# Performance work log

Hardware: AMD Instinct MI355X
Metric: run time of the kernel (lower is better)

The kernel has to match this reference:

```python
import jax, jax.numpy as jnp
import numpy as np

N_POI = 100000   # number of POIs
N_EDGE = 50000   # directed hyperedges
N_USER = 50000   # user hyperedges (multi-view)
NNZ = 1_000_000  # nonzeros per incidence matrix
D = 128          # embedding dim
L = 3            # num_layers


def spmm(rows, cols, vals, x, num_rows):
    """COO sparse @ dense: y[r] += vals * x[c]."""
    return jax.ops.segment_sum(vals[:, None] * x[cols], rows, num_segments=num_rows)


def hyper_net(pois, rows1, cols1, vals1, n1, rows2, cols2, vals2, n2, attn):
    """Chained two-hop sparse propagation with relu + residual, layer-attention fusion.
    Dropout omitted (eval mode / deterministic reference)."""
    embs = [pois]
    x = pois
    for _ in range(L):
        m = spmm(rows1, cols1, vals1, x, n1)      # [n1, D] aggregate to hyperedges/users
        m = spmm(rows2, cols2, vals2, m, n2)      # [N_POI, D] propagate back to POIs
        x = jax.nn.relu(m) + embs[-1]             # relu + residual
        embs.append(x)
    w = jax.nn.softmax(attn)                      # [L+1]
    return jnp.einsum('l,lnd->nd', w, jnp.stack(embs))


def setup_inputs() -> dict:
    key = jax.random.key(0)
    ks = jax.random.split(key, 16)
    inp = {
        'pois_embs': jax.random.normal(ks[0], (N_POI, D), dtype=jnp.float32),
        'tar_rows': jax.random.randint(ks[1], (NNZ,), 0, N_EDGE, dtype=jnp.int32),
        'tar_cols': jax.random.randint(ks[2], (NNZ,), 0, N_POI, dtype=jnp.int32),
        'tar_vals': jax.random.uniform(ks[3], (NNZ,), dtype=jnp.float32),
        'src_rows': jax.random.randint(ks[4], (NNZ,), 0, N_POI, dtype=jnp.int32),
        'src_cols': jax.random.randint(ks[5], (NNZ,), 0, N_EDGE, dtype=jnp.int32),
        'src_vals': jax.random.uniform(ks[6], (NNZ,), dtype=jnp.float32),
        'up_rows': jax.random.randint(ks[7], (NNZ,), 0, N_USER, dtype=jnp.int32),
        'up_cols': jax.random.randint(ks[8], (NNZ,), 0, N_POI, dtype=jnp.int32),
        'up_vals': jax.random.uniform(ks[9], (NNZ,), dtype=jnp.float32),
        'pu_rows': jax.random.randint(ks[10], (NNZ,), 0, N_POI, dtype=jnp.int32),
        'pu_cols': jax.random.randint(ks[11], (NNZ,), 0, N_USER, dtype=jnp.int32),
        'pu_vals': jax.random.uniform(ks[12], (NNZ,), dtype=jnp.float32),
        'attn_di': jnp.ones((L + 1,), dtype=jnp.float32),
        'attn_mv': jnp.ones((L + 1,), dtype=jnp.float32),
    }
    return inp


def reference(pois_embs, tar_rows, tar_cols, tar_vals, src_rows, src_cols, src_vals,
              up_rows, up_cols, up_vals, pu_rows, pu_cols, pu_vals, attn_di, attn_mv):
    # Directed hypergraph branch: msg_tar = HG_poi_tar @ x ; msg_src = HG_poi_src @ msg_tar
    di = hyper_net(pois_embs, tar_rows, tar_cols, tar_vals, N_EDGE,
                   src_rows, src_cols, src_vals, N_POI, attn_di)
    # Multi-view (user) hypergraph branch: HG_up @ x ; HG_pu @ msg
    mv = hyper_net(pois_embs, up_rows, up_cols, up_vals, N_USER,
                   pu_rows, pu_cols, pu_vals, N_POI, attn_mv)
    return di + mv
```

## Files before the change

kernel.cpp:

```cpp
#include <hip/hip_runtime.h>

#define NNZC   1000000
#define NPOI   100000
#define NEDGE  50000
#define NUSER  50000
#define DIM    128
#define NL     3

#define PB     64
#define NBKT   196
#define SCANN  (4 * NBKT * PB)

static inline int ceil_div(int a, int b) { return (a + b - 1) / b; }

typedef unsigned int uint32;

__device__ __forceinline__ float bfLO(uint32 u) { return __uint_as_float(u << 16); }
__device__ __forceinline__ float bfHI(uint32 u) { return __uint_as_float(u & 0xffff0000u); }
__device__ __forceinline__ uint32 bf16_rne(float f) {
    uint32 u = __float_as_uint(f);
    return (u + 0x7fffu + ((u >> 16) & 1u)) >> 16;
}
__device__ __forceinline__ uint32 bfPACK(float a, float b) {
    return bf16_rne(a) | (bf16_rne(b) << 16);
}
__device__ __forceinline__ uint32 csrPACK(int col, float val) {
    return ((uint32)col) | (bf16_rne(val) << 17);
}
__device__ __forceinline__ int   csrCOL(uint32 e) { return (int)(e & 0x1FFFFu); }
__device__ __forceinline__ float csrVAL(uint32 e) { return __uint_as_float((e >> 17) << 16); }

__device__ __constant__ const int c_nrows[4]  = { NEDGE, NPOI, NUSER, NPOI };
__device__ __constant__ const int c_cntoff[4] = { 0, NEDGE, NEDGE + NPOI, NEDGE + NPOI + NUSER };
__device__ __constant__ const int c_cap[4]    = { 64, 48, 64, 48 };
__device__ __constant__ const int c_shift[4]  = { 8, 9, 8, 9 };
__device__ __constant__ const long long c_elloff[4] = { 0, 3200000, 8000000, 11200000 };


__global__ __launch_bounds__(1024) void histH_kernel(
    const int* __restrict__ r0, const int* __restrict__ r1,
    const int* __restrict__ r2, const int* __restrict__ r3,
    int* __restrict__ histG) {
    __shared__ int h[NBKT];
    int m = blockIdx.y, p = blockIdx.x;
    for (int i = threadIdx.x; i < NBKT; i += 1024) h[i] = 0;
    __syncthreads();
    const int* r = (m == 0) ? r0 : (m == 1) ? r1 : (m == 2) ? r2 : r3;
    int shift = c_shift[m];
    int lo = (int)(((long long)NNZC * p) >> 6);
    int hi = (int)(((long long)NNZC * (p + 1)) >> 6);
    for (int i = lo + (int)threadIdx.x; i < hi; i += 1024)
        atomicAdd(&h[r[i] >> shift], 1);
    __syncthreads();
    for (int b = threadIdx.x; b < NBKT; b += 1024)
        histG[(m * NBKT + b) * PB + p] = h[b];
}

__global__ __launch_bounds__(256) void scan_kernel(int* __restrict__ g) {
    __shared__ int base[257];
    int t = threadIdx.x;
    const int chunk = SCANN / 256;
    int lo = t * chunk;
    int s = 0;
    for (int i = 0; i < chunk; i++) s += g[lo + i];
    base[t + 1] = s;
    __syncthreads();
    if (t == 0) {
        base[0] = 0;
        for (int i = 1; i <= 256; i++) base[i] += base[i - 1];
    }
    __syncthreads();
    int off = base[t];
    for (int i = 0; i < chunk; i++) { int v = g[lo + i]; g[lo + i] = off; off += v; }
    if (t == 255) g[SCANN] = base[256];
}

__global__ __launch_bounds__(1024) void scatS_kernel(
    const int* __restrict__ r0, const int* __restrict__ r1,
    const int* __restrict__ r2, const int* __restrict__ r3,
    const int* __restrict__ c0, const int* __restrict__ c1,
    const int* __restrict__ c2, const int* __restrict__ c3,
    const float* __restrict__ v0, const float* __restrict__ v1,
    const float* __restrict__ v2, const float* __restrict__ v3,
    const int* __restrict__ scanG, uint2* __restrict__ rec) {
    __shared__ int cur[NBKT];
    int m = blockIdx.y, p = blockIdx.x;
    for (int b = threadIdx.x; b < NBKT; b += 1024)
        cur[b] = scanG[(m * NBKT + b) * PB + p];
    __syncthreads();
    const int*   r = (m == 0) ? r0 : (m == 1) ? r1 : (m == 2) ? r2 : r3;
    const int*   c = (m == 0) ? c0 : (m == 1) ? c1 : (m == 2) ? c2 : c3;
    const float* v = (m == 0) ? v0 : (m == 1) ? v1 : (m == 2) ? v2 : v3;
    int shift = c_shift[m];
    int lo = (int)(((long long)NNZC * p) >> 6);
    int hi = (int)(((long long)NNZC * (p + 1)) >> 6);
    for (int i = lo + (int)threadIdx.x; i < hi; i += 1024) {
        int row = r[i];
        int pos = atomicAdd(&cur[row >> shift], 1);
        rec[pos] = make_uint2((uint32)row, csrPACK(c[i], v[i]));
    }
}

__global__ __launch_bounds__(512) void fillB_kernel(
    const int* __restrict__ scanG, const uint2* __restrict__ rec,
    int* __restrict__ counts_all, uint32* __restrict__ ell) {
    __shared__ int cnt[512];
    int bx = (int)blockIdx.x;
    int m = bx / NBKT, b = bx - m * NBKT;
    int shift = c_shift[m];
    int rowlo = b << shift;
    int bklen = 1 << shift;
    for (int i = threadIdx.x; i < bklen; i += 512) cnt[i] = 0;
    __syncthreads();
    int lo = scanG[(m * NBKT + b) * PB];
    int hi = scanG[(m * NBKT + b + 1) * PB];
    int cap = c_cap[m];
    uint32* ebase = ell + c_elloff[m];
    for (int i = lo + (int)threadIdx.x; i < hi; i += 512) {
        uint2 e = rec[i];
        int row = (int)e.x;
        int pos = atomicAdd(&cnt[row - rowlo], 1);
        ebase[(size_t)row * cap + pos] = e.y;
    }
    __syncthreads();
    int nrows_b = c_nrows[m] - rowlo;
    if (nrows_b > bklen) nrows_b = bklen;
    int* counts = counts_all + c_cntoff[m];
    for (int i = threadIdx.x; i < nrows_b; i += 512) {
        int ci = cnt[i];
        counts[rowlo + i] = ci;
        int pad = (ci + 7) & ~7;
        uint32* erow = ebase + (size_t)(rowlo + i) * cap;
        for (int j = ci; j < pad; j++) erow[j] = 0;
    }
}

__global__ __launch_bounds__(256) void cast_soft_kernel(
    const float* __restrict__ src, uint32* __restrict__ dst,
    const float* __restrict__ adi, const float* __restrict__ amv,
    float* __restrict__ w) {
    int bx = (int)blockIdx.x;
    if (bx < 25000) {
        int i = bx * 256 + (int)threadIdx.x;
        float2 f = *(const float2*)(src + (size_t)i * 2);
        dst[i] = bfPACK(f.x, f.y);
        return;
    }
    if (threadIdx.x == 0) {
        for (int b = 0; b < 2; b++) {
            const float* a = b ? amv : adi;
            float m = a[0];
            for (int l = 1; l < 4; l++) m = fmaxf(m, a[l]);
            float e[4]; float s = 0.f;
            for (int l = 0; l < 4; l++) { e[l] = __expf(a[l] - m); s += e[l]; }
            for (int l = 0; l < 4; l++) w[b * 4 + l] = e[l] / s;
        }
    }
}

__device__ __forceinline__ void fma8(float2& a0, float2& a1, float2& a2, float2& a3,
                                     float v, uint4 u) {
    a0.x = fmaf(v, bfLO(u.x), a0.x); a0.y = fmaf(v, bfHI(u.x), a0.y);
    a1.x = fmaf(v, bfLO(u.y), a1.x); a1.y = fmaf(v, bfHI(u.y), a1.y);
    a2.x = fmaf(v, bfLO(u.z), a2.x); a2.y = fmaf(v, bfHI(u.z), a2.y);
    a3.x = fmaf(v, bfLO(u.w), a3.x); a3.y = fmaf(v, bfHI(u.w), a3.y);
}

template<int CAP>
__global__ __launch_bounds__(256) void spmm1_kernel(
    const int* __restrict__ counts, const uint32* __restrict__ ell,
    const uint32* __restrict__ xbf, uint32* __restrict__ ybf, int n_rows) {
    int row = (int)((blockIdx.x * blockDim.x + threadIdx.x) >> 4);
    int t   = (int)(threadIdx.x & 15);
    if (row >= n_rows) return;
    int pad = (counts[row] + 7) & ~7;
    const uint32* erow = ell + (size_t)row * CAP;
    float2 a0 = {0.f,0.f}, a1 = {0.f,0.f}, a2 = {0.f,0.f}, a3 = {0.f,0.f};
    for (int j = 0; j < pad; j += 8) {
        uint4 qa = *(const uint4*)(erow + j);
        uint4 qb = *(const uint4*)(erow + j + 4);
        uint4 u0 = *((const uint4*)(xbf + (size_t)csrCOL(qa.x) * 64) + t);
        uint4 u1 = *((const uint4*)(xbf + (size_t)csrCOL(qa.y) * 64) + t);
        uint4 u2 = *((const uint4*)(xbf + (size_t)csrCOL(qa.z) * 64) + t);
        uint4 u3 = *((const uint4*)(xbf + (size_t)csrCOL(qa.w) * 64) + t);
        uint4 u4 = *((const uint4*)(xbf + (size_t)csrCOL(qb.x) * 64) + t);
        uint4 u5 = *((const uint4*)(xbf + (size_t)csrCOL(qb.y) * 64) + t);
        uint4 u6 = *((const uint4*)(xbf + (size_t)csrCOL(qb.z) * 64) + t);
        uint4 u7 = *((const uint4*)(xbf + (size_t)csrCOL(qb.w) * 64) + t);
        fma8(a0,a1,a2,a3, csrVAL(qa.x), u0); fma8(a0,a1,a2,a3, csrVAL(qa.y), u1);
        fma8(a0,a1,a2,a3, csrVAL(qa.z), u2); fma8(a0,a1,a2,a3, csrVAL(qa.w), u3);
        fma8(a0,a1,a2,a3, csrVAL(qb.x), u4); fma8(a0,a1,a2,a3, csrVAL(qb.y), u5);
        fma8(a0,a1,a2,a3, csrVAL(qb.z), u6); fma8(a0,a1,a2,a3, csrVAL(qb.w), u7);
    }
    uint4 o;
    o.x = bfPACK(a0.x, a0.y); o.y = bfPACK(a1.x, a1.y);
    o.z = bfPACK(a2.x, a2.y); o.w = bfPACK(a3.x, a3.y);
    *((uint4*)(ybf + (size_t)row * 64) + t) = o;
}

template<int CAP, int MODE>
__global__ __launch_bounds__(256) void spmm2_kernel(
    const int* __restrict__ counts, const uint32* __restrict__ ell,
    const uint32* __restrict__ mbf, const uint32* __restrict__ xinbf,
    uint32* __restrict__ xoutbf, const uint32* __restrict__ x1bf,
    const float* __restrict__ pois, const float* __restrict__ w,
    float* __restrict__ outf, int n_rows) {
    int row = (int)((blockIdx.x * blockDim.x + threadIdx.x) >> 4);
    int t   = (int)(threadIdx.x & 15);
    if (row >= n_rows) return;
    int pad = (counts[row] + 7) & ~7;
    const uint32* erow = ell + (size_t)row * CAP;
    float2 a0 = {0.f,0.f}, a1 = {0.f,0.f}, a2 = {0.f,0.f}, a3 = {0.f,0.f};
    for (int j = 0; j < pad; j += 8) {
        uint4 qa = *(const uint4*)(erow + j);
        uint4 qb = *(const uint4*)(erow + j + 4);
        uint4 u0 = *((const uint4*)(mbf + (size_t)csrCOL(qa.x) * 64) + t);
        uint4 u1 = *((const uint4*)(mbf + (size_t)csrCOL(qa.y) * 64) + t);
        uint4 u2 = *((const uint4*)(mbf + (size_t)csrCOL(qa.z) * 64) + t);
        uint4 u3 = *((const uint4*)(mbf + (size_t)csrCOL(qa.w) * 64) + t);
        uint4 u4 = *((const uint4*)(mbf + (size_t)csrCOL(qb.x) * 64) + t);
        uint4 u5 = *((const uint4*)(mbf + (size_t)csrCOL(qb.y) * 64) + t);
        uint4 u6 = *((const uint4*)(mbf + (size_t)csrCOL(qb.z) * 64) + t);
        uint4 u7 = *((const uint4*)(mbf + (size_t)csrCOL(qb.w) * 64) + t);
        fma8(a0,a1,a2,a3, csrVAL(qa.x), u0); fma8(a0,a1,a2,a3, csrVAL(qa.y), u1);
        fma8(a0,a1,a2,a3, csrVAL(qa.z), u2); fma8(a0,a1,a2,a3, csrVAL(qa.w), u3);
        fma8(a0,a1,a2,a3, csrVAL(qb.x), u4); fma8(a0,a1,a2,a3, csrVAL(qb.y), u5);
        fma8(a0,a1,a2,a3, csrVAL(qb.z), u6); fma8(a0,a1,a2,a3, csrVAL(qb.w), u7);
    }
    uint4 ui = *((const uint4*)(xinbf + (size_t)row * 64) + t);
    float x2v[8] = { bfLO(ui.x), bfHI(ui.x), bfLO(ui.y), bfHI(ui.y),
                     bfLO(ui.z), bfHI(ui.z), bfLO(ui.w), bfHI(ui.w) };
    float x3v[8] = { fmaxf(a0.x,0.f)+x2v[0], fmaxf(a0.y,0.f)+x2v[1],
                     fmaxf(a1.x,0.f)+x2v[2], fmaxf(a1.y,0.f)+x2v[3],
                     fmaxf(a2.x,0.f)+x2v[4], fmaxf(a2.y,0.f)+x2v[5],
                     fmaxf(a3.x,0.f)+x2v[6], fmaxf(a3.y,0.f)+x2v[7] };
    if (MODE == 0) {
        uint4 o;
        o.x = bfPACK(x3v[0], x3v[1]); o.y = bfPACK(x3v[2], x3v[3]);
        o.z = bfPACK(x3v[4], x3v[5]); o.w = bfPACK(x3v[6], x3v[7]);
        *((uint4*)(xoutbf + (size_t)row * 64) + t) = o;
    } else {
        uint4 u1v = *((const uint4*)(x1bf + (size_t)row * 64) + t);
        float x1v[8] = { bfLO(u1v.x), bfHI(u1v.x), bfLO(u1v.y), bfHI(u1v.y),
                         bfLO(u1v.z), bfHI(u1v.z), bfLO(u1v.w), bfHI(u1v.w) };
        float* op = outf + (size_t)row * 128 + t * 8;
        float4 o0, o1;
        if (MODE == 1) {
            float w04 = w[0] + w[4];
            const float* pp = pois + (size_t)row * 128 + t * 8;
            float4 p0 = ((const float4*)pp)[0], p1 = ((const float4*)pp)[1];
            o0.x = w04*p0.x + w[1]*x1v[0] + w[2]*x2v[0] + w[3]*x3v[0];
            o0.y = w04*p0.y + w[1]*x1v[1] + w[2]*x2v[1] + w[3]*x3v[1];
            o0.z = w04*p0.z + w[1]*x1v[2] + w[2]*x2v[2] + w[3]*x3v[2];
            o0.w = w04*p0.w + w[1]*x1v[3] + w[2]*x2v[3] + w[3]*x3v[3];
            o1.x = w04*p1.x + w[1]*x1v[4] + w[2]*x2v[4] + w[3]*x3v[4];
            o1.y = w04*p1.y + w[1]*x1v[5] + w[2]*x2v[5] + w[3]*x3v[5];
            o1.z = w04*p1.z + w[1]*x1v[6] + w[2]*x2v[6] + w[3]*x3v[6];
            o1.w = w04*p1.w + w[1]*x1v[7] + w[2]*x2v[7] + w[3]*x3v[7];
        } else {
            float4 p0 = ((const float4*)op)[0], p1 = ((const float4*)op)[1];
            o0.x = p0.x + w[5]*x1v[0] + w[6]*x2v[0] + w[7]*x3v[0];
            o0.y = p0.y + w[5]*x1v[1] + w[6]*x2v[1] + w[7]*x3v[1];
            o0.z = p0.z + w[5]*x1v[2] + w[6]*x2v[2] + w[7]*x3v[2];
            o0.w = p0.w + w[5]*x1v[3] + w[6]*x2v[3] + w[7]*x3v[3];
            o1.x = p1.x + w[5]*x1v[4] + w[6]*x2v[4] + w[7]*x3v[4];
            o1.y = p1.y + w[5]*x1v[5] + w[6]*x2v[5] + w[7]*x3v[5];
            o1.z = p1.z + w[5]*x1v[6] + w[6]*x2v[6] + w[7]*x3v[6];
            o1.w = p1.w + w[5]*x1v[7] + w[6]*x2v[7] + w[7]*x3v[7];
        }
        ((float4*)op)[0] = o0;
        ((float4*)op)[1] = o1;
    }
}

extern "C" void kernel_launch(void* const* d_in, const int* in_sizes, int n_in,
                              void* d_out, int out_size, void* d_ws, size_t ws_size,
                              hipStream_t stream) {
    const float* pois = (const float*)d_in[0];
    const int*   rows_in[4] = { (const int*)d_in[1], (const int*)d_in[4],
                                (const int*)d_in[7], (const int*)d_in[10] };
    const int*   cols_in[4] = { (const int*)d_in[2], (const int*)d_in[5],
                                (const int*)d_in[8], (const int*)d_in[11] };
    const float* vals_in[4] = { (const float*)d_in[3], (const float*)d_in[6],
                                (const float*)d_in[9], (const float*)d_in[12] };
    const float* attn_di = (const float*)d_in[13];
    const float* attn_mv = (const float*)d_in[14];
    float* out = (float*)d_out;

    const int cnt_off[4] = { 0, NEDGE, NEDGE + NPOI, NEDGE + NPOI + NUSER };
    const long long ell_off[4] = { 0, 3200000, 8000000, 11200000 };
    const int NTOT = NEDGE + NPOI + NUSER + NPOI;

    char* p = (char*)d_ws;
    float*  wsoft      = (float*)p;  p += 256;
    int*    counts_all = (int*)p;    p += (size_t)NTOT * 4;
    p = (char*)(((size_t)p + 255) & ~255ull);
    int*    scanG      = (int*)p;    p += (size_t)(SCANN + 64) * 4;
    p = (char*)(((size_t)p + 255) & ~255ull);
    uint32* ell        = (uint32*)p; p += (size_t)16000000 * 4;
    uint32* mbf        = (uint32*)p; p += (size_t)NEDGE * 64 * 4;
    uint32* poisbf     = (uint32*)p; p += (size_t)NPOI * 64 * 4;
    uint32* xl[3];
    for (int l = 0; l < 3; l++) { xl[l] = (uint32*)p; p += (size_t)NPOI * 64 * 4; }
    uint2* rec = (uint2*)xl[0];
    (void)ws_size; (void)out_size; (void)n_in; (void)in_sizes;

    histH_kernel<<<dim3(PB, 4), 1024, 0, stream>>>(
        rows_in[0], rows_in[1], rows_in[2], rows_in[3], scanG);
    scan_kernel<<<1, 256, 0, stream>>>(scanG);
    scatS_kernel<<<dim3(PB, 4), 1024, 0, stream>>>(
        rows_in[0], rows_in[1], rows_in[2], rows_in[3],
        cols_in[0], cols_in[1], cols_in[2], cols_in[3],
        vals_in[0], vals_in[1], vals_in[2], vals_in[3],
        scanG, rec);
    fillB_kernel<<<4 * NBKT, 512, 0, stream>>>(scanG, rec, counts_all, ell);

    cast_soft_kernel<<<25000 + 1, 256, 0, stream>>>(pois, poisbf, attn_di, attn_mv, wsoft);

    for (int br = 0; br < 2; br++) {
        int m1i = br ? 2 : 0;
        int m2i = br ? 3 : 1;
        const int* cn1 = counts_all + cnt_off[m1i];
        const int* cn2 = counts_all + cnt_off[m2i];
        const uint32* el1 = ell + ell_off[m1i];
        const uint32* el2 = ell + ell_off[m2i];
        const int n1 = 50000;
        const uint32* xcur = poisbf;
        for (int l = 1; l <= NL; l++) {
            spmm1_kernel<64><<<ceil_div(n1, 16), 256, 0, stream>>>(cn1, el1, xcur, mbf, n1);
            if (l < NL) {
                spmm2_kernel<48, 0><<<ceil_div(NPOI, 16), 256, 0, stream>>>(
                    cn2, el2, mbf, xcur, xl[l - 1], nullptr, nullptr, wsoft, nullptr, NPOI);
                xcur = xl[l - 1];
            } else if (br == 0) {
                spmm2_kernel<48, 1><<<ceil_div(NPOI, 16), 256, 0, stream>>>(
                    cn2, el2, mbf, xcur, nullptr, xl[0], pois, wsoft, out, NPOI);
            } else {
                spmm2_kernel<48, 2><<<ceil_div(NPOI, 16), 256, 0, stream>>>(
                    cn2, el2, mbf, xcur, nullptr, xl[0], nullptr, wsoft, out, NPOI);
            }
        }
    }
}
```

Before: 736.0 us.

## Merge both hypergraph branches into single SpMM launches per layer

Runs the directed and multi-view branches together: each layer does one spmm1 launch over both edge sets and one spmm2 launch over both POI sets. The final layer fuses both branches' second hop and the attention combine into one kernel, so out is written once and never read back. The pu column indices are offset at CSR build time so both branches gather from one merged message buffer. This cuts the number of launches and doubles the work per launch, which should fill the GPU better and remove the read-modify-write of out. It needs more workspace, so a fallback path for smaller workspaces is kept. The final kernel now reads pois as bf16 rather than fp32, which adds some rounding to the output.

```diff
diff --git a/kernel.cpp b/kernel.cpp
--- a/kernel.cpp
+++ b/kernel.cpp
@@ -34,6 +34,7 @@
 __device__ __constant__ const int c_cntoff[4] = { 0, NEDGE, NEDGE + NPOI, NEDGE + NPOI + NUSER };
 __device__ __constant__ const int c_cap[4]    = { 64, 48, 64, 48 };
 __device__ __constant__ const int c_shift[4]  = { 8, 9, 8, 9 };
+__device__ __constant__ const int c_coloff[4] = { 0, 0, 0, 50000 };
 __device__ __constant__ const long long c_elloff[4] = { 0, 3200000, 8000000, 11200000 };
 
 
@@ -92,12 +93,13 @@
     const int*   c = (m == 0) ? c0 : (m == 1) ? c1 : (m == 2) ? c2 : c3;
     const float* v = (m == 0) ? v0 : (m == 1) ? v1 : (m == 2) ? v2 : v3;
     int shift = c_shift[m];
+    int coff  = c_coloff[m];
     int lo = (int)(((long long)NNZC * p) >> 6);
     int hi = (int)(((long long)NNZC * (p + 1)) >> 6);
     for (int i = lo + (int)threadIdx.x; i < hi; i += 1024) {
         int row = r[i];
         int pos = atomicAdd(&cur[row >> shift], 1);
-        rec[pos] = make_uint2((uint32)row, csrPACK(c[i], v[i]));
+        rec[pos] = make_uint2((uint32)row, csrPACK(c[i] + coff, v[i]));
     }
 }
 
@@ -165,112 +167,153 @@
     a2.x = fmaf(v, bfLO(u.z), a2.x); a2.y = fmaf(v, bfHI(u.z), a2.y);
     a3.x = fmaf(v, bfLO(u.w), a3.x); a3.y = fmaf(v, bfHI(u.w), a3.y);
 }
-
-template<int CAP>
-__global__ __launch_bounds__(256) void spmm1_kernel(
-    const int* __restrict__ counts, const uint32* __restrict__ ell,
-    const uint32* __restrict__ xbf, uint32* __restrict__ ybf, int n_rows) {
-    int row = (int)((blockIdx.x * blockDim.x + threadIdx.x) >> 4);
-    int t   = (int)(threadIdx.x & 15);
-    if (row >= n_rows) return;
-    int pad = (counts[row] + 7) & ~7;
-    const uint32* erow = ell + (size_t)row * CAP;
-    float2 a0 = {0.f,0.f}, a1 = {0.f,0.f}, a2 = {0.f,0.f}, a3 = {0.f,0.f};
+__device__ __forceinline__ void gather8(const uint32* __restrict__ erow, int pad,
+                                        const uint32* __restrict__ x, int t,
+                                        float2& a0, float2& a1, float2& a2, float2& a3) {
     for (int j = 0; j < pad; j += 8) {
         uint4 qa = *(const uint4*)(erow + j);
         uint4 qb = *(const uint4*)(erow + j + 4);
-        uint4 u0 = *((const uint4*)(xbf + (size_t)csrCOL(qa.x) * 64) + t);
-        uint4 u1 = *((const uint4*)(xbf + (size_t)csrCOL(qa.y) * 64) + t);
-        uint4 u2 = *((const uint4*)(xbf + (size_t)csrCOL(qa.z) * 64) + t);
-        uint4 u3 = *((const uint4*)(xbf + (size_t)csrCOL(qa.w) * 64) + t);
-        uint4 u4 = *((const uint4*)(xbf + (size_t)csrCOL(qb.x) * 64) + t);
-        uint4 u5 = *((const uint4*)(xbf + (size_t)csrCOL(qb.y) * 64) + t);
-        uint4 u6 = *((const uint4*)(xbf + (size_t)csrCOL(qb.z) * 64) + t);
-        uint4 u7 = *((const uint4*)(xbf + (size_t)csrCOL(qb.w) * 64) + t);
+        uint4 u0 = *((const uint4*)(x + (size_t)csrCOL(qa.x) * 64) + t);
+        uint4 u1 = *((const uint4*)(x + (size_t)csrCOL(qa.y) * 64) + t);
+        uint4 u2 = *((const uint4*)(x + (size_t)csrCOL(qa.z) * 64) + t);
+        uint4 u3 = *((const uint4*)(x + (size_t)csrCOL(qa.w) * 64) + t);
+        uint4 u4 = *((const uint4*)(x + (size_t)csrCOL(qb.x) * 64) + t);
+        uint4 u5 = *((const uint4*)(x + (size_t)csrCOL(qb.y) * 64) + t);
+        uint4 u6 = *((const uint4*)(x + (size_t)csrCOL(qb.z) * 64) + t);
+        uint4 u7 = *((const uint4*)(x + (size_t)csrCOL(qb.w) * 64) + t);
         fma8(a0,a1,a2,a3, csrVAL(qa.x), u0); fma8(a0,a1,a2,a3, csrVAL(qa.y), u1);
         fma8(a0,a1,a2,a3, csrVAL(qa.z), u2); fma8(a0,a1,a2,a3, csrVAL(qa.w), u3);
         fma8(a0,a1,a2,a3, csrVAL(qb.x), u4); fma8(a0,a1,a2,a3, csrVAL(qb.y), u5);
         fma8(a0,a1,a2,a3, csrVAL(qb.z), u6); fma8(a0,a1,a2,a3, csrVAL(qb.w), u7);
     }
+}
+__device__ __forceinline__ void unp8(uint4 u, float* o) {
+    o[0]=bfLO(u.x); o[1]=bfHI(u.x); o[2]=bfLO(u.y); o[3]=bfHI(u.y);
+    o[4]=bfLO(u.z); o[5]=bfHI(u.z); o[6]=bfLO(u.w); o[7]=bfHI(u.w);
+}
+
+__global__ __launch_bounds__(256) void spmm1M_kernel(
+    const int* __restrict__ cntA, const uint32* __restrict__ ellA, const uint32* __restrict__ xA,
+    const int* __restrict__ cntB, const uint32* __restrict__ ellB, const uint32* __restrict__ xB,
+    uint32* __restrict__ ybf, int n0, int ntot) {
+    int row = (int)((blockIdx.x * blockDim.x + threadIdx.x) >> 4);
+    int t   = (int)(threadIdx.x & 15);
+    if (row >= ntot) return;
+    const int* cnt; const uint32* ell; const uint32* x; int lr;
+    if (row < n0) { cnt = cntA; ell = ellA; x = xA; lr = row; }
+    else          { cnt = cntB; ell = ellB; x = xB; lr = row - n0; }
+    int pad = (cnt[lr] + 7) & ~7;
+    const uint32* erow = ell + (size_t)lr * 64;
+    float2 a0 = {0.f,0.f}, a1 = {0.f,0.f}, a2 = {0.f,0.f}, a3 = {0.f,0.f};
+    gather8(erow, pad, x, t, a0, a1, a2, a3);
     uint4 o;
     o.x = bfPACK(a0.x, a0.y); o.y = bfPACK(a1.x, a1.y);
     o.z = bfPACK(a2.x, a2.y); o.w = bfPACK(a3.x, a3.y);
     *((uint4*)(ybf + (size_t)row * 64) + t) = o;
 }
 
-template<int CAP, int MODE>
-__global__ __launch_bounds__(256) void spmm2_kernel(
-    const int* __restrict__ counts, const uint32* __restrict__ ell,
-    const uint32* __restrict__ mbf, const uint32* __restrict__ xinbf,
-    uint32* __restrict__ xoutbf, const uint32* __restrict__ x1bf,
-    const float* __restrict__ pois, const float* __restrict__ w,
-    float* __restrict__ outf, int n_rows) {
+__global__ __launch_bounds__(256) void spmm2M_kernel(
+    const int* __restrict__ cntA, const uint32* __restrict__ ellA,
+    const uint32* __restrict__ xinA, uint32* __restrict__ xoutA,
+    const int* __restrict__ cntB, const uint32* __restrict__ ellB,
+    const uint32* __restrict__ xinB, uint32* __restrict__ xoutB,
+    const uint32* __restrict__ gbase, int n0, int ntot) {
     int row = (int)((blockIdx.x * blockDim.x + threadIdx.x) >> 4);
     int t   = (int)(threadIdx.x & 15);
-    if (row >= n_rows) return;
-    int pad = (counts[row] + 7) & ~7;
-    const uint32* erow = ell + (size_t)row * CAP;
+    if (row >= ntot) return;
+    const int* cnt; const uint32* ell; const uint32* xin; uint32* xout; int lr;
+    if (row < n0) { cnt = cntA; ell = ellA; xin = xinA; xout = xoutA; lr = row; }
+    else          { cnt = cntB; ell = ellB; xin = xinB; xout = xoutB; lr = row - n0; }
+    int pad = (cnt[lr] + 7) & ~7;
+    const uint32* erow = ell + (size_t)lr * 48;
     float2 a0 = {0.f,0.f}, a1 = {0.f,0.f}, a2 = {0.f,0.f}, a3 = {0.f,0.f};
-    for (int j = 0; j < pad; j += 8) {
-        uint4 qa = *(const uint4*)(erow + j);
-        uint4 qb = *(const uint4*)(erow + j + 4);
-        uint4 u0 = *((const uint4*)(mbf + (size_t)csrCOL(qa.x) * 64) + t);
-        uint4 u1 = *((const uint4*)(mbf + (size_t)csrCOL(qa.y) * 64) + t);
-        uint4 u2 = *((const uint4*)(mbf + (size_t)csrCOL(qa.z) * 64) + t);
-        uint4 u3 = *((const uint4*)(mbf + (size_t)csrCOL(qa.w) * 64) + t);
-        uint4 u4 = *((const uint4*)(mbf + (size_t)csrCOL(qb.x) * 64) + t);
-        uint4 u5 = *((const uint4*)(mbf + (size_t)csrCOL(qb.y) * 64) + t);
-        uint4 u6 = *((const uint4*)(mbf + (size_t)csrCOL(qb.z) * 64) + t);
-        uint4 u7 = *((const uint4*)(mbf + (size_t)csrCOL(qb.w) * 64) + t);
-        fma8(a0,a1,a2,a3, csrVAL(qa.x), u0); fma8(a0,a1,a2,a3, csrVAL(qa.y), u1);
-        fma8(a0,a1,a2,a3, csrVAL(qa.z), u2); fma8(a0,a1,a2,a3, csrVAL(qa.w), u3);
-        fma8(a0,a1,a2,a3, csrVAL(qb.x), u4); fma8(a0,a1,a2,a3, csrVAL(qb.y), u5);
-        fma8(a0,a1,a2,a3, csrVAL(qb.z), u6); fma8(a0,a1,a2,a3, csrVAL(qb.w), u7);
-    }
-    uint4 ui = *((const uint4*)(xinbf + (size_t)row * 64) + t);
-    float x2v[8] = { bfLO(ui.x), bfHI(ui.x), bfLO(ui.y), bfHI(ui.y),
-                     bfLO(ui.z), bfHI(ui.z), bfLO(ui.w), bfHI(ui.w) };
+    gather8(erow, pad, gbase, t, a0, a1, a2, a3);
+    uint4 ui = *((const uint4*)(xin + (size_t)lr * 64) + t);
+    float xi[8]; unp8(ui, xi);
+    uint4 o;
+    o.x = bfPACK(fmaxf(a0.x,0.f)+xi[0], fmaxf(a0.y,0.f)+xi[1]);
+    o.y = bfPACK(fmaxf(a1.x,0.f)+xi[2], fmaxf(a1.y,0.f)+xi[3]);
+    o.z = bfPACK(fmaxf(a2.x,0.f)+xi[4], fmaxf(a2.y,0.f)+xi[5]);
+    o.w = bfPACK(fmaxf(a3.x,0.f)+xi[6], fmaxf(a3.y,0.f)+xi[7]);
+    *((uint4*)(xout + (size_t)lr * 64) + t) = o;
+}
+
+__global__ __launch_bounds__(256) void spmm2F_kernel(
+    const int* __restrict__ cntS, const uint32* __restrict__ ellS,
+    const int* __restrict__ cntP, const uint32* __restrict__ ellP,
+    const uint32* __restrict__ gbase,
+    const uint32* __restrict__ x1A, const uint32* __restrict__ x2A,
+    const uint32* __restrict__ x1B, const uint32* __restrict__ x2B,
+    const uint32* __restrict__ poisbf, const float* __restrict__ w,
+    float* __restrict__ out, int n) {
+    int row = (int)((blockIdx.x * blockDim.x + threadIdx.x) >> 4);
+    int t   = (int)(threadIdx.x & 15);
+    if (row >= n) return;
+    float2 a0={0,0}, a1={0,0}, a2={0,0}, a3={0,0};
+    gather8(ellS + (size_t)row * 48, (cntS[row] + 7) & ~7, gbase, t, a0, a1, a2, a3);
+    float x2a[8]; unp8(*((const uint4*)(x2A + (size_t)row * 64) + t), x2a);
+    float x3a[8] = { fmaxf(a0.x,0.f)+x2a[0], fmaxf(a0.y,0.f)+x2a[1],
+                     fmaxf(a1.x,0.f)+x2a[2], fmaxf(a1.y,0.f)+x2a[3],
+                     fmaxf(a2.x,0.f)+x2a[4], fmaxf(a2.y,0.f)+x2a[5],
+                     fmaxf(a3.x,0.f)+x2a[6], fmaxf(a3.y,0.f)+x2a[7] };
+    a0={0,0}; a1={0,0}; a2={0,0}; a3={0,0};
+    gather8(ellP + (size_t)row * 48, (cntP[row] + 7) & ~7, gbase, t, a0, a1, a2, a3);
+    float x2b[8]; unp8(*((const uint4*)(x2B + (size_t)row * 64) + t), x2b);
+    float x3b[8] = { fmaxf(a0.x,0.f)+x2b[0], fmaxf(a0.y,0.f)+x2b[1],
+                     fmaxf(a1.x,0.f)+x2b[2], fmaxf(a1.y,0.f)+x2b[3],
+                     fmaxf(a2.x,0.f)+x2b[4], fmaxf(a2.y,0.f)+x2b[5],
+                     fmaxf(a3.x,0.f)+x2b[6], fmaxf(a3.y,0.f)+x2b[7] };
+    float x1a[8]; unp8(*((const uint4*)(x1A + (size_t)row * 64) + t), x1a);
+    float x1b[8]; unp8(*((const uint4*)(x1B + (size_t)row * 64) + t), x1b);
+    float pv[8];  unp8(*((const uint4*)(poisbf + (size_t)row * 64) + t), pv);
+    float w04 = w[0] + w[4];
+    float* op = out + (size_t)row * 128 + t * 8;
+    float4 o0, o1;
+    float ov[8];
+#pragma unroll
+    for (int k = 0; k < 8; k++)
+        ov[k] = w04*pv[k] + w[1]*x1a[k] + w[2]*x2a[k] + w[3]*x3a[k]
+                          + w[5]*x1b[k] + w[6]*x2b[k] + w[7]*x3b[k];
+    o0 = make_float4(ov[0], ov[1], ov[2], ov[3]);
+    o1 = make_float4(ov[4], ov[5], ov[6], ov[7]);
+    ((float4*)op)[0] = o0;
+    ((float4*)op)[1] = o1;
+}
+
+template<int MODE>
+__global__ __launch_bounds__(256) void spmm2E_kernel(
+    const int* __restrict__ counts, const uint32* __restrict__ ell,
+    const uint32* __restrict__ gbase, const uint32* __restrict__ xinbf,
+    const uint32* __restrict__ x1bf, const uint32* __restrict__ poisbf,
+    const float* __restrict__ w, float* __restrict__ out, int n) {
+    int row = (int)((blockIdx.x * blockDim.x + threadIdx.x) >> 4);
+    int t   = (int)(threadIdx.x & 15);
+    if (row >= n) return;
+    float2 a0={0,0}, a1={0,0}, a2={0,0}, a3={0,0};
+    gather8(ell + (size_t)row * 48, (counts[row] + 7) & ~7, gbase, t, a0, a1, a2, a3);
+    float x2v[8]; unp8(*((const uint4*)(xinbf + (size_t)row * 64) + t), x2v);
     float x3v[8] = { fmaxf(a0.x,0.f)+x2v[0], fmaxf(a0.y,0.f)+x2v[1],
                      fmaxf(a1.x,0.f)+x2v[2], fmaxf(a1.y,0.f)+x2v[3],
                      fmaxf(a2.x,0.f)+x2v[4], fmaxf(a2.y,0.f)+x2v[5],
                      fmaxf(a3.x,0.f)+x2v[6], fmaxf(a3.y,0.f)+x2v[7] };
-    if (MODE == 0) {
-        uint4 o;
-        o.x = bfPACK(x3v[0], x3v[1]); o.y = bfPACK(x3v[2], x3v[3]);
-        o.z = bfPACK(x3v[4], x3v[5]); o.w = bfPACK(x3v[6], x3v[7]);
-        *((uint4*)(xoutbf + (size_t)row * 64) + t) = o;
+    float x1v[8]; unp8(*((const uint4*)(x1bf + (size_t)row * 64) + t), x1v);
+    float* op = out + (size_t)row * 128 + t * 8;
+    float ov[8];
+    if (MODE == 1) {
+        float pv[8]; unp8(*((const uint4*)(poisbf + (size_t)row * 64) + t), pv);
+        float w04 = w[0] + w[4];
+#pragma unroll
+        for (int k = 0; k < 8; k++)
+            ov[k] = w04*pv[k] + w[1]*x1v[k] + w[2]*x2v[k] + w[3]*x3v[k];
     } else {
-        uint4 u1v = *((const uint4*)(x1bf + (size_t)row * 64) + t);
-        float x1v[8] = { bfLO(u1v.x), bfHI(u1v.x), bfLO(u1v.y), bfHI(u1v.y),
-                         bfLO(u1v.z), bfHI(u1v.z), bfLO(u1v.w), bfHI(u1v.w) };
-        float* op = outf + (size_t)row * 128 + t * 8;
-        float4 o0, o1;
-        if (MODE == 1) {
-            float w04 = w[0] + w[4];
-            const float* pp = pois + (size_t)row * 128 + t * 8;
-            float4 p0 = ((const float4*)pp)[0], p1 = ((const float4*)pp)[1];
-            o0.x = w04*p0.x + w[1]*x1v[0] + w[2]*x2v[0] + w[3]*x3v[0];
-            o0.y = w04*p0.y + w[1]*x1v[1] + w[2]*x2v[1] + w[3]*x3v[1];
-            o0.z = w04*p0.z + w[1]*x1v[2] + w[2]*x2v[2] + w[3]*x3v[2];
-            o0.w = w04*p0.w + w[1]*x1v[3] + w[2]*x2v[3] + w[3]*x3v[3];
-            o1.x = w04*p1.x + w[1]*x1v[4] + w[2]*x2v[4] + w[3]*x3v[4];
-            o1.y = w04*p1.y + w[1]*x1v[5] + w[2]*x2v[5] + w[3]*x3v[5];
-            o1.z = w04*p1.z + w[1]*x1v[6] + w[2]*x2v[6] + w[3]*x3v[6];
-            o1.w = w04*p1.w + w[1]*x1v[7] + w[2]*x2v[7] + w[3]*x3v[7];
-        } else {
-            float4 p0 = ((const float4*)op)[0], p1 = ((const float4*)op)[1];
-            o0.x = p0.x + w[5]*x1v[0] + w[6]*x2v[0] + w[7]*x3v[0];
-            o0.y = p0.y + w[5]*x1v[1] + w[6]*x2v[1] + w[7]*x3v[1];
-            o0.z = p0.z + w[5]*x1v[2] + w[6]*x2v[2] + w[7]*x3v[2];
-            o0.w = p0.w + w[5]*x1v[3] + w[6]*x2v[3] + w[7]*x3v[3];
-            o1.x = p1.x + w[5]*x1v[4] + w[6]*x2v[4] + w[7]*x3v[4];
-            o1.y = p1.y + w[5]*x1v[5] + w[6]*x2v[5] + w[7]*x3v[5];
-            o1.z = p1.z + w[5]*x1v[6] + w[6]*x2v[6] + w[7]*x3v[6];
-            o1.w = p1.w + w[5]*x1v[7] + w[6]*x2v[7] + w[7]*x3v[7];
-        }
-        ((float4*)op)[0] = o0;
-        ((float4*)op)[1] = o1;
-    }
+        float4 p0 = ((const float4*)op)[0], p1 = ((const float4*)op)[1];
+        float pr[8] = { p0.x,p0.y,p0.z,p0.w, p1.x,p1.y,p1.z,p1.w };
+#pragma unroll
+        for (int k = 0; k < 8; k++)
+            ov[k] = pr[k] + w[5]*x1v[k] + w[6]*x2v[k] + w[7]*x3v[k];
+    }
+    ((float4*)op)[0] = make_float4(ov[0], ov[1], ov[2], ov[3]);
+    ((float4*)op)[1] = make_float4(ov[4], ov[5], ov[6], ov[7]);
 }
 
 extern "C" void kernel_launch(void* const* d_in, const int* in_sizes, int n_in,
@@ -290,21 +333,22 @@
     const int cnt_off[4] = { 0, NEDGE, NEDGE + NPOI, NEDGE + NPOI + NUSER };
     const long long ell_off[4] = { 0, 3200000, 8000000, 11200000 };
     const int NTOT = NEDGE + NPOI + NUSER + NPOI;
-
-    char* p = (char*)d_ws;
+    const size_t XB = (size_t)NPOI * 64 * 4;
+
+    char* base = (char*)d_ws;
+    char* p = base;
     float*  wsoft      = (float*)p;  p += 256;
     int*    counts_all = (int*)p;    p += (size_t)NTOT * 4;
     p = (char*)(((size_t)p + 255) & ~255ull);
     int*    scanG      = (int*)p;    p += (size_t)(SCANN + 64) * 4;
     p = (char*)(((size_t)p + 255) & ~255ull);
     uint32* ell        = (uint32*)p; p += (size_t)16000000 * 4;
-    uint32* mbf        = (uint32*)p; p += (size_t)NEDGE * 64 * 4;
-    uint32* poisbf     = (uint32*)p; p += (size_t)NPOI * 64 * 4;
-    uint32* xl[3];
-    for (int l = 0; l < 3; l++) { xl[l] = (uint32*)p; p += (size_t)NPOI * 64 * 4; }
-    uint2* rec = (uint2*)xl[0];
-    (void)ws_size; (void)out_size; (void)n_in; (void)in_sizes;
-
+    uint32* poisbf     = (uint32*)p; p += XB;
+    char*   varp       = p;
+
+    bool merged = ((size_t)(varp - base) + 5 * XB) <= ws_size;
+
+    uint2* rec = (uint2*)varp;
     histH_kernel<<<dim3(PB, 4), 1024, 0, stream>>>(
         rows_in[0], rows_in[1], rows_in[2], rows_in[3], scanG);
     scan_kernel<<<1, 256, 0, stream>>>(scanG);
@@ -314,31 +358,67 @@
         vals_in[0], vals_in[1], vals_in[2], vals_in[3],
         scanG, rec);
     fillB_kernel<<<4 * NBKT, 512, 0, stream>>>(scanG, rec, counts_all, ell);
-
     cast_soft_kernel<<<25000 + 1, 256, 0, stream>>>(pois, poisbf, attn_di, attn_mv, wsoft);
 
-    for (int br = 0; br < 2; br++) {
-        int m1i = br ? 2 : 0;
-        int m2i = br ? 3 : 1;
-        const int* cn1 = counts_all + cnt_off[m1i];
-        const int* cn2 = counts_all + cnt_off[m2i];
-        const uint32* el1 = ell + ell_off[m1i];
-        const uint32* el2 = ell + ell_off[m2i];
-        const int n1 = 50000;
-        const uint32* xcur = poisbf;
+    const int* cn_tar = counts_all + cnt_off[0];
+    const int* cn_src = counts_all + cnt_off[1];
+    const int* cn_up  = counts_all + cnt_off[2];
+    const int* cn_pu  = counts_all + cnt_off[3];
+    const uint32* el_tar = ell + ell_off[0];
+    const uint32* el_src = ell + ell_off[1];
+    const uint32* el_up  = ell + ell_off[2];
+    const uint32* el_pu  = ell + ell_off[3];
+
+    if (merged) {
+        uint32* mbfM = (uint32*)varp;
+        uint32* xA1  = (uint32*)(varp + 1 * XB);
+        uint32* xA2  = (uint32*)(varp + 2 * XB);
+        uint32* xB1  = (uint32*)(varp + 3 * XB);
+        uint32* xB2  = (uint32*)(varp + 4 * XB);
+        const uint32* xa = poisbf; const uint32* xb = poisbf;
         for (int l = 1; l <= NL; l++) {
-            spmm1_kernel<64><<<ceil_div(n1, 16), 256, 0, stream>>>(cn1, el1, xcur, mbf, n1);
+            spmm1M_kernel<<<ceil_div(2 * NEDGE, 16), 256, 0, stream>>>(
+                cn_tar, el_tar, xa, cn_up, el_up, xb, mbfM, NEDGE, 2 * NEDGE);
             if (l < NL) {
-                spmm2_kernel<48, 0><<<ceil_div(NPOI, 16), 256, 0, stream>>>(
-                    cn2, el2, mbf, xcur, xl[l - 1], nullptr, nullptr, wsoft, nullptr, NPOI);
-                xcur = xl[l - 1];
-            } else if (br == 0) {
-                spmm2_kernel<48, 1><<<ceil_div(NPOI, 16), 256, 0, stream>>>(
-                    cn2, el2, mbf, xcur, nullptr, xl[0], pois, wsoft, out, NPOI);
+                uint32* xoa = (l == 1) ? xA1 : xA2;
+                uint32* xob = (l == 1) ? xB1 : xB2;
+                spmm2M_kernel<<<ceil_div(2 * NPOI, 16), 256, 0, stream>>>(
+                    cn_src, el_src, xa, xoa, cn_pu, el_pu, xb, xob, mbfM, NPOI, 2 * NPOI);
+                xa = xoa; xb = xob;
             } else {
-                spmm2_kernel<48, 2><<<ceil_div(NPOI, 16), 256, 0, stream>>>(
-                    cn2, el2, mbf, xcur, nullptr, xl[0], nullptr, wsoft, out, NPOI);
+                spmm2F_kernel<<<ceil_div(NPOI, 16), 256, 0, stream>>>(
+                    cn_src, el_src, cn_pu, el_pu, mbfM,
+                    xA1, xA2, xB1, xB2, poisbf, wsoft, out, NPOI);
             }
         }
-    }
-}
+    } else {
+        uint32* mbf = (uint32*)varp;
+        uint32* xl0 = (uint32*)(varp + XB / 2);
+        uint32* xl1 = (uint32*)(varp + XB / 2 + XB);
+        const uint32* mbf_pu = mbf - (size_t)NEDGE * 64;
+        for (int br = 0; br < 2; br++) {
+            const int* cn1 = br ? cn_up : cn_tar;
+            const int* cn2 = br ? cn_pu : cn_src;
+            const uint32* el1 = br ? el_up : el_tar;
+            const uint32* el2 = br ? el_pu : el_src;
+            const uint32* gb  = br ? mbf_pu : mbf;
+            const uint32* xcur = poisbf;
+            for (int l = 1; l <= NL; l++) {
+                spmm1M_kernel<<<ceil_div(NEDGE, 16), 256, 0, stream>>>(
+                    cn1, el1, xcur, cn1, el1, xcur, mbf, NEDGE, NEDGE);
+                if (l < NL) {
+                    uint32* xo = (l == 1) ? xl0 : xl1;
+                    spmm2M_kernel<<<ceil_div(NPOI, 16), 256, 0, stream>>>(
+                        cn2, el2, xcur, xo, cn2, el2, xcur, xo, gb, NPOI, NPOI);
+                    xcur = xo;
+                } else if (br == 0) {
+                    spmm2E_kernel<1><<<ceil_div(NPOI, 16), 256, 0, stream>>>(
+                        cn2, el2, gb, xcur, xl0, poisbf, wsoft, out, NPOI);
+                } else {
+                    spmm2E_kernel<2><<<ceil_div(NPOI, 16), 256, 0, stream>>>(
+                        cn2, el2, gb, xcur, xl0, poisbf, wsoft, out, NPOI);
+                }
+            }
+        }
+    }
+}
```

Result: faster. 699.1 us (-5.0%).
